# Performance work log

Hardware: AMD Instinct MI355X
Metric: run time of the kernel (lower is better)

## Reference

```python
import jax, jax.numpy as jnp
import numpy as np

V, DM, DEPTH, N = 50257, 512, 8, 16  # vocab, dim, depth, ssm_dim
B, L = 2, 1024
GATE = 0.5  # fixed_gate=True blend


def layer_norm(x, g, b):
    mu = x.mean(-1, keepdims=True)
    xm = x - mu
    var = (xm * xm).mean(-1, keepdims=True)
    return xm * jax.lax.rsqrt(var + 1e-5) * g + b


def ssm(u, W_dt, b_dt, W_B, W_C, A_log, D_p):
    # selective SSM: h_t = exp(dt_t*A)*h_{t-1} + dt_t*B_t*u_t ; y_t = C_t.h_t + D*u_t
    dt = jax.nn.softplus(u @ W_dt + b_dt)            # (B,L,DM)
    Bm = u @ W_B                                      # (B,L,N)
    Cm = u @ W_C                                      # (B,L,N)
    A = -jnp.exp(A_log)                               # (DM,N), stable (negative)

    def step(h, inp):
        dt_t, B_t, C_t, u_t = inp                     # (B,DM),(B,N),(B,N),(B,DM)
        h = jnp.exp(dt_t[..., None] * A) * h + (dt_t * u_t)[..., None] * B_t[:, None, :]
        y = jnp.einsum('bdn,bn->bd', h, C_t)
        return h, y

    h0 = jnp.zeros((u.shape[0], DM, N), u.dtype)
    xs = (dt.transpose(1, 0, 2), Bm.transpose(1, 0, 2), Cm.transpose(1, 0, 2), u.transpose(1, 0, 2))
    _, ys = jax.lax.scan(step, h0, xs)
    return ys.transpose(1, 0, 2) + D_p * u


def wkv(x, W_r, W_k, W_v, W_o, t_decay, t_first):
    # RWKV-4 channel-wise WKV recurrence
    r = jax.nn.sigmoid(x @ W_r)
    k = jnp.clip(x @ W_k, -30.0, 30.0)
    v = x @ W_v
    w = jnp.exp(-jnp.exp(t_decay))                    # (DM,) decay in (0,1)

    def step(carry, inp):
        a, b = carry
        k_t, v_t = inp
        ek = jnp.exp(k_t)
        eu = jnp.exp(t_first + k_t)
        out = (a + eu * v_t) / (b + eu + 1e-6)
        return (w * a + ek * v_t, w * b + ek), out

    a0 = jnp.zeros((x.shape[0], DM), x.dtype)
    _, o = jax.lax.scan(step, (a0, jnp.zeros_like(a0)), (k.transpose(1, 0, 2), v.transpose(1, 0, 2)))
    return (r * o.transpose(1, 0, 2)) @ W_o


def setup_inputs() -> dict:
    key = jax.random.key(0)
    ks = jax.random.split(key, 16)
    s = 0.02
    inp = {
        'input_ids': jax.random.randint(ks[0], (B, L), 0, V, dtype=jnp.int32),
        'emb': jax.random.normal(ks[1], (V, DM), jnp.float32) * s,
        'ln1_g': jnp.ones((DEPTH, DM), jnp.float32),
        'ln1_b': jnp.zeros((DEPTH, DM), jnp.float32),
        'W_dt': jax.random.normal(ks[2], (DEPTH, DM, DM), jnp.float32) * s,
        'b_dt': jnp.zeros((DEPTH, DM), jnp.float32),
        'W_B': jax.random.normal(ks[3], (DEPTH, DM, N), jnp.float32) * s,
        'W_C': jax.random.normal(ks[4], (DEPTH, DM, N), jnp.float32) * s,
        'A_log': jnp.broadcast_to(jnp.log(jnp.arange(1, N + 1, dtype=jnp.float32)), (DEPTH, DM, N)).copy(),
        'D_p': jnp.ones((DEPTH, DM), jnp.float32),
        'ln2_g': jnp.ones((DEPTH, DM), jnp.float32),
        'ln2_b': jnp.zeros((DEPTH, DM), jnp.float32),
        'W_r': jax.random.normal(ks[5], (DEPTH, DM, DM), jnp.float32) * s,
        'W_k': jax.random.normal(ks[6], (DEPTH, DM, DM), jnp.float32) * s,
        'W_v': jax.random.normal(ks[7], (DEPTH, DM, DM), jnp.float32) * s,
        'W_o': jax.random.normal(ks[8], (DEPTH, DM, DM), jnp.float32) * s,
        't_decay': jax.random.normal(ks[9], (DEPTH, DM), jnp.float32) * 0.5,
        't_first': jax.random.normal(ks[10], (DEPTH, DM), jnp.float32) * 0.5,
        'lnf_g': jnp.ones((DM,), jnp.float32),
        'lnf_b': jnp.zeros((DM,), jnp.float32),
    }
    return inp


def reference(input_ids, emb, ln1_g, ln1_b, W_dt, b_dt, W_B, W_C, A_log, D_p,
              ln2_g, ln2_b, W_r, W_k, W_v, W_o, t_decay, t_first, lnf_g, lnf_b):
    x = emb[input_ids]                                # (B,L,DM)
    for i in range(DEPTH):
        x = x + GATE * ssm(layer_norm(x, ln1_g[i], ln1_b[i]),
                           W_dt[i], b_dt[i], W_B[i], W_C[i], A_log[i], D_p[i])
        x = x + GATE * wkv(layer_norm(x, ln2_g[i], ln2_b[i]),
                           W_r[i], W_k[i], W_v[i], W_o[i], t_decay[i], t_first[i])
    x = layer_norm(x, lnf_g, lnf_b)
    logits = x @ emb.T                                # tied LM head, (B,L,V)
    return logits
```

## Files before the change

kernel.cpp:

```cpp
#include <hip/hip_runtime.h>

#define DM 512
#define NST 16
#define NDEPTH 8
#define NB 2
#define NL 1024
#define MROWS 2048
#define VOCAB 50257
#define VPAD  50304
#define NCH 64
#define CLEN 16

typedef __attribute__((ext_vector_type(8))) short bf16x8;
typedef __attribute__((ext_vector_type(4))) float f32x4;
typedef __attribute__((ext_vector_type(8))) unsigned short ushort8;

#define AS1(p) ((const __attribute__((address_space(1))) void*)(p))
#define AS3(p) ((__attribute__((address_space(3))) void*)(p))

static __device__ __forceinline__ unsigned short f2bf(float f) {
  unsigned int x = __float_as_uint(f);
  unsigned int r = (x + 0x7FFFu + ((x >> 16) & 1u)) >> 16;
  return (unsigned short)r;
}

__global__ __launch_bounds__(256) void k_gather(const int* __restrict__ ids,
    const float* __restrict__ emb, float* __restrict__ x)
{
  int gid = blockIdx.x * 256 + threadIdx.x;
  int row = gid >> 7, c = (gid & 127) * 4;
  int id = ids[row];
  *(float4*)(x + (size_t)row * DM + c) = *(const float4*)(emb + (size_t)id * DM + c);
}

__global__ void k_transpose(const float* __restrict__ Wdt, const float* __restrict__ Wr,
    const float* __restrict__ Wk, const float* __restrict__ Wv, const float* __restrict__ Wo,
    unsigned short* __restrict__ Tdtbc, unsigned short* __restrict__ Trkv, unsigned short* __restrict__ To)
{
  __shared__ float tile[32][33];
  int z = blockIdx.z, layer = z / 5, f = z % 5;
  const float* src;
  unsigned short* dst;
  size_t lw = (size_t)layer * DM * DM;
  if (f == 0)      { src = Wdt + lw; dst = Tdtbc + (size_t)layer * 640 * DM; }
  else if (f == 1) { src = Wr  + lw; dst = Trkv + (size_t)layer * 3 * DM * DM; }
  else if (f == 2) { src = Wk  + lw; dst = Trkv + (size_t)layer * 3 * DM * DM + DM * DM; }
  else if (f == 3) { src = Wv  + lw; dst = Trkv + (size_t)layer * 3 * DM * DM + 2 * DM * DM; }
  else             { src = Wo  + lw; dst = To   + lw; }
  int tx = threadIdx.x, ty = threadIdx.y;
  int kb = blockIdx.y * 32, nb = blockIdx.x * 32;
  #pragma unroll
  for (int i = 0; i < 4; i++)
    tile[ty + i * 8][tx] = src[(size_t)(kb + ty + i * 8) * DM + nb + tx];
  __syncthreads();
  #pragma unroll
  for (int i = 0; i < 4; i++)
    dst[(size_t)(nb + ty + i * 8) * DM + kb + tx] = f2bf(tile[tx][ty + i * 8]);
}

__global__ __launch_bounds__(256) void k_bcpack(const float* __restrict__ WB,
    const float* __restrict__ WC, unsigned short* __restrict__ Tdtbc)
{
  int gid = blockIdx.x * 256 + threadIdx.x;
  int k = gid & 511, n = (gid >> 9) & 127, layer = gid >> 16;
  float v = 0.f;
  if (n < 16)      v = WB[((size_t)layer * DM + k) * NST + n];
  else if (n < 32) v = WC[((size_t)layer * DM + k) * NST + (n - 16)];
  Tdtbc[(size_t)layer * 640 * DM + (size_t)(512 + n) * DM + k] = f2bf(v);
}

__global__ __launch_bounds__(256) void k_embcvt(const float* __restrict__ emb,
    unsigned short* __restrict__ out)
{
  int gid = blockIdx.x * 256 + threadIdx.x;
  size_t base = (size_t)gid * 8;
  int row = (int)(base >> 9);
  ushort8 o;
  if (row < VOCAB) {
    float4 a = *(const float4*)(emb + base);
    float4 b = *(const float4*)(emb + base + 4);
    o[0]=f2bf(a.x); o[1]=f2bf(a.y); o[2]=f2bf(a.z); o[3]=f2bf(a.w);
    o[4]=f2bf(b.x); o[5]=f2bf(b.y); o[6]=f2bf(b.z); o[7]=f2bf(b.w);
  } else {
    o = (ushort8)0;
  }
  *(ushort8*)(out + base) = o;
}

__global__ __launch_bounds__(256) void k_ln(const float* __restrict__ x,
    const float* __restrict__ g, const float* __restrict__ bb,
    float* __restrict__ of, unsigned short* __restrict__ ob)
{
  const int w = threadIdx.x >> 6, l = threadIdx.x & 63;
  const int row = blockIdx.x * 4 + w;
  const float* xr = x + (size_t)row * DM + l * 8;
  float4 v0 = *(const float4*)(xr);
  float4 v1 = *(const float4*)(xr + 4);
  float s = v0.x + v0.y + v0.z + v0.w + v1.x + v1.y + v1.z + v1.w;
  float q = v0.x*v0.x + v0.y*v0.y + v0.z*v0.z + v0.w*v0.w
          + v1.x*v1.x + v1.y*v1.y + v1.z*v1.z + v1.w*v1.w;
  #pragma unroll
  for (int m = 1; m < 64; m <<= 1) { s += __shfl_xor(s, m); q += __shfl_xor(q, m); }
  const float mu = s * (1.0f / DM);
  const float var = q * (1.0f / DM) - mu * mu;
  const float rs = rsqrtf(var + 1e-5f);
  const float4 g0 = *(const float4*)(g + l * 8);
  const float4 g1 = *(const float4*)(g + l * 8 + 4);
  const float4 b0 = *(const float4*)(bb + l * 8);
  const float4 b1 = *(const float4*)(bb + l * 8 + 4);
  float y[8];
  y[0] = (v0.x - mu) * rs * g0.x + b0.x;
  y[1] = (v0.y - mu) * rs * g0.y + b0.y;
  y[2] = (v0.z - mu) * rs * g0.z + b0.z;
  y[3] = (v0.w - mu) * rs * g0.w + b0.w;
  y[4] = (v1.x - mu) * rs * g1.x + b1.x;
  y[5] = (v1.y - mu) * rs * g1.y + b1.y;
  y[6] = (v1.z - mu) * rs * g1.z + b1.z;
  y[7] = (v1.w - mu) * rs * g1.w + b1.w;
  if (of) {
    float4 o0 = {y[0], y[1], y[2], y[3]}, o1 = {y[4], y[5], y[6], y[7]};
    *(float4*)(of + (size_t)row * DM + l * 8) = o0;
    *(float4*)(of + (size_t)row * DM + l * 8 + 4) = o1;
  }
  if (ob) {
    ushort8 o;
    #pragma unroll
    for (int j = 0; j < 8; j++) o[j] = f2bf(y[j]);
    *(ushort8*)(ob + (size_t)row * DM + l * 8) = o;
  }
}

__global__ __launch_bounds__(256) void gemm_head(const unsigned short* __restrict__ A,
    const unsigned short* __restrict__ Bt, float* __restrict__ C, int N)
{
  constexpr int K = DM;
  __shared__ unsigned short lsA[128 * 32];
  __shared__ unsigned short lsB[128 * 32];
  const int t = threadIdx.x;
  const int w = t >> 6, l = t & 63;
  const int wm = (w >> 1) * 64, wn = (w & 1) * 64;
  const int per = gridDim.x >> 3;
  const int wg = ((int)blockIdx.x & 7) * per + ((int)blockIdx.x >> 3);
  const size_t bm = (size_t)(wg & 15) * 128, bn = (size_t)(wg >> 4) * 128;
  f32x4 acc[4][4] = {};
  const int r0 = t >> 2, c0 = (t & 3) * 8;
  const unsigned short* Ab = A + (bm + r0) * K + c0;
  const unsigned short* Bb = Bt + (bn + r0) * K + c0;
  const int lr = l & 15, lk = (l >> 4) * 8;
  for (int k0 = 0; k0 < K; k0 += 32) {
    __builtin_amdgcn_global_load_lds(AS1(Ab + k0),          AS3(lsA + t * 8),        16, 0, 0);
    __builtin_amdgcn_global_load_lds(AS1(Ab + 64 * K + k0), AS3(lsA + 2048 + t * 8), 16, 0, 0);
    __builtin_amdgcn_global_load_lds(AS1(Bb + k0),          AS3(lsB + t * 8),        16, 0, 0);
    __builtin_amdgcn_global_load_lds(AS1(Bb + 64 * K + k0), AS3(lsB + 2048 + t * 8), 16, 0, 0);
    asm volatile("s_waitcnt vmcnt(0)" ::: "memory");
    __syncthreads();
    bf16x8 af[4], bfr[4];
    #pragma unroll
    for (int i = 0; i < 4; i++) af[i]  = *(const bf16x8*)(lsA + (wm + i * 16 + lr) * 32 + lk);
    #pragma unroll
    for (int i = 0; i < 4; i++) bfr[i] = *(const bf16x8*)(lsB + (wn + i * 16 + lr) * 32 + lk);
    #pragma unroll
    for (int mi = 0; mi < 4; mi++)
      #pragma unroll
      for (int ni = 0; ni < 4; ni++)
        acc[mi][ni] = __builtin_amdgcn_mfma_f32_16x16x32_bf16(af[mi], bfr[ni], acc[mi][ni], 0, 0, 0);
    __syncthreads();
  }
  const int lg = l >> 4;
  #pragma unroll
  for (int mi = 0; mi < 4; mi++) {
    #pragma unroll
    for (int ni = 0; ni < 4; ni++) {
      int n = (int)bn + wn + ni * 16 + lr;
      if (n >= N) continue;
      size_t m0 = bm + wm + mi * 16 + lg * 4;
      #pragma unroll
      for (int j = 0; j < 4; j++)
        C[(m0 + j) * (size_t)N + n] = acc[mi][ni][j];
    }
  }
}

template<int EPI>
__global__ __launch_bounds__(256) void gemm64(const unsigned short* __restrict__ A,
    const unsigned short* __restrict__ Bt, float* __restrict__ C, int ldc,
    const float* __restrict__ bias, float* __restrict__ C2)
{
  constexpr int K = DM;
  __shared__ unsigned short lsA[64 * 32];
  __shared__ unsigned short lsB[128 * 32];
  const int t = threadIdx.x;
  const int w = t >> 6, l = t & 63;
  const int wm = (w >> 1) * 32, wn = (w & 1) * 64;
  const size_t bm = (size_t)blockIdx.x * 64, bn = (size_t)blockIdx.y * 128;
  f32x4 acc[2][4] = {};
  const int r0 = t >> 2, c0 = (t & 3) * 8;
  const unsigned short* Ab = A + (bm + r0) * K + c0;
  const unsigned short* Bb = Bt + (bn + r0) * K + c0;
  const int lr = l & 15, lk = (l >> 4) * 8;
  for (int k0 = 0; k0 < K; k0 += 32) {
    __builtin_amdgcn_global_load_lds(AS1(Ab + k0),          AS3(lsA + t * 8),        16, 0, 0);
    __builtin_amdgcn_global_load_lds(AS1(Bb + k0),          AS3(lsB + t * 8),        16, 0, 0);
    __builtin_amdgcn_global_load_lds(AS1(Bb + 64 * K + k0), AS3(lsB + 2048 + t * 8), 16, 0, 0);
    asm volatile("s_waitcnt vmcnt(0)" ::: "memory");
    __syncthreads();
    bf16x8 af[2], bfr[4];
    #pragma unroll
    for (int i = 0; i < 2; i++) af[i]  = *(const bf16x8*)(lsA + (wm + i * 16 + lr) * 32 + lk);
    #pragma unroll
    for (int i = 0; i < 4; i++) bfr[i] = *(const bf16x8*)(lsB + (wn + i * 16 + lr) * 32 + lk);
    #pragma unroll
    for (int mi = 0; mi < 2; mi++)
      #pragma unroll
      for (int ni = 0; ni < 4; ni++)
        acc[mi][ni] = __builtin_amdgcn_mfma_f32_16x16x32_bf16(af[mi], bfr[ni], acc[mi][ni], 0, 0, 0);
    __syncthreads();
  }
  const int lg = l >> 4;
  #pragma unroll
  for (int mi = 0; mi < 2; mi++) {
    #pragma unroll
    for (int ni = 0; ni < 4; ni++) {
      int n = (int)bn + wn + ni * 16 + lr;
      size_t m0 = bm + wm + mi * 16 + lg * 4;
      #pragma unroll
      for (int j = 0; j < 4; j++) {
        float v = acc[mi][ni][j];
        if (EPI == 0) {
          C[(m0 + j) * (size_t)ldc + n] = v;
        } else if (EPI == 2) {
          C2[(m0 + j) * (size_t)ldc + n] += 0.5f * v;
        } else {
          if (n < 512) {
            float b = v + bias[n];
            C[(m0 + j) * (size_t)512 + n] = fmaxf(b, 0.f) + log1pf(__expf(-fabsf(b)));
          } else if (n < 544) {
            C2[(m0 + j) * (size_t)32 + (n - 512)] = v;
          }
        }
      }
    }
  }
}

__global__ __launch_bounds__(256) void k_ssm1(const float* __restrict__ dt,
    const float* __restrict__ u, const float* __restrict__ BC,
    const float* __restrict__ A_log, float* __restrict__ Pb, float* __restrict__ Sb)
{
  const int t = threadIdx.x;
  const int grp = t >> 4, n = t & 15;
  const int cg = blockIdx.x & 63, ck = blockIdx.x >> 6;
  const int ch = cg * 16 + grp;
  const int b = ch >> 9, d = ch & 511;
  const float A = -__expf(A_log[d * NST + n]);
  const int t0 = ck * CLEN;
  const float* dtp = dt + ((size_t)b * NL + t0) * DM + d;
  const float* up  = u  + ((size_t)b * NL + t0) * DM + d;
  const float* bcp = BC + ((size_t)b * NL + t0) * 32 + n;
  float P = 1.f, S = 0.f;
  #pragma unroll
  for (int tt = 0; tt < CLEN; ++tt) {
    float dtv = dtp[(size_t)tt * DM];
    float uv  = up[(size_t)tt * DM];
    float Bv  = bcp[(size_t)tt * 32];
    float e = __expf(dtv * A);
    S = fmaf(e, S, dtv * uv * Bv);
    P *= e;
  }
  size_t cn = (size_t)ch * NST + n;
  Pb[cn * NCH + ck] = P;
  Sb[cn * NCH + ck] = S;
}

__global__ __launch_bounds__(256) void k_ssm2(const float* __restrict__ Pb,
    const float* __restrict__ Sb, float* __restrict__ H0)
{
  const int wid = blockIdx.x * 4 + (threadIdx.x >> 6);
  const int lane = threadIdx.x & 63;
  float coef = Pb[(size_t)wid * NCH + lane];
  float sum  = Sb[(size_t)wid * NCH + lane];
  #pragma unroll
  for (int m = 1; m < 64; m <<= 1) {
    float cr = __shfl_up(coef, m);
    float sr = __shfl_up(sum, m);
    if (lane >= m) { sum = fmaf(coef, sr, sum); coef *= cr; }
  }
  float hp = __shfl_up(sum, 1);
  H0[(size_t)wid * NCH + lane] = (lane == 0) ? 0.f : hp;
}

__global__ __launch_bounds__(256) void k_ssm3(const float* __restrict__ dt,
    const float* __restrict__ u, const float* __restrict__ BC,
    const float* __restrict__ A_log, const float* __restrict__ Dp,
    const float* __restrict__ H0, float* __restrict__ x)
{
  const int t = threadIdx.x;
  const int grp = t >> 4, n = t & 15;
  const int cg = blockIdx.x & 63, ck = blockIdx.x >> 6;
  const int ch = cg * 16 + grp;
  const int b = ch >> 9, d = ch & 511;
  const float A = -__expf(A_log[d * NST + n]);
  const float Dpv = Dp[d];
  const int t0 = ck * CLEN;
  const float* dtp = dt + ((size_t)b * NL + t0) * DM + d;
  const float* up  = u  + ((size_t)b * NL + t0) * DM + d;
  const float* bcp = BC + ((size_t)b * NL + t0) * 32 + n;
  float* xp = x + ((size_t)b * NL + t0) * DM + d;
  size_t cn = (size_t)ch * NST + n;
  float h = H0[cn * NCH + ck];
  #pragma unroll
  for (int tt = 0; tt < CLEN; ++tt) {
    float dtv = dtp[(size_t)tt * DM];
    float uv  = up[(size_t)tt * DM];
    float Bv  = bcp[(size_t)tt * 32];
    float Cv  = bcp[(size_t)tt * 32 + 16];
    float e = __expf(dtv * A);
    h = fmaf(e, h, dtv * uv * Bv);
    float p2 = h * Cv;
    p2 += __shfl_xor(p2, 1);
    p2 += __shfl_xor(p2, 2);
    p2 += __shfl_xor(p2, 4);
    p2 += __shfl_xor(p2, 8);
    if (n == 0) xp[(size_t)tt * DM] += 0.5f * (p2 + Dpv * uv);
  }
}

__global__ __launch_bounds__(256) void k_wkv1(const float* __restrict__ rkv,
    const float* __restrict__ tdec, float* __restrict__ SaB, float* __restrict__ SbB)
{
  const int gid = blockIdx.x * 256 + threadIdx.x;
  const int ch = gid & 1023, ck = gid >> 10;
  const int b = ch >> 9, d = ch & 511;
  const float w = __expf(-__expf(tdec[d]));
  const float* base = rkv + ((size_t)b * NL + ck * CLEN) * 1536;
  float Sa = 0.f, Sb = 0.f;
  #pragma unroll
  for (int tt = 0; tt < CLEN; ++tt) {
    const float* row = base + (size_t)tt * 1536;
    float kt = row[512 + d];
    kt = fminf(30.f, fmaxf(-30.f, kt));
    float vt = row[1024 + d];
    float ek = __expf(kt);
    Sa = fmaf(w, Sa, ek * vt);
    Sb = fmaf(w, Sb, ek);
  }
  SaB[(size_t)ch * NCH + ck] = Sa;
  SbB[(size_t)ch * NCH + ck] = Sb;
}

__global__ __launch_bounds__(256) void k_wkv2(const float* __restrict__ SaB,
    const float* __restrict__ SbB, const float* __restrict__ tdec,
    float* __restrict__ HaB, float* __restrict__ HbB)
{
  const int ch = blockIdx.x * 4 + (threadIdx.x >> 6);
  const int lane = threadIdx.x & 63;
  const int d = ch & 511;
  float coef = __expf(-16.f * __expf(tdec[d]));
  float sa = SaB[(size_t)ch * NCH + lane];
  float sb = SbB[(size_t)ch * NCH + lane];
  #pragma unroll
  for (int m = 1; m < 64; m <<= 1) {
    float cr  = __shfl_up(coef, m);
    float sar = __shfl_up(sa, m);
    float sbr = __shfl_up(sb, m);
    if (lane >= m) { sa = fmaf(coef, sar, sa); sb = fmaf(coef, sbr, sb); coef *= cr; }
  }
  float ha = __shfl_up(sa, 1);
  float hb = __shfl_up(sb, 1);
  HaB[(size_t)ch * NCH + lane] = (lane == 0) ? 0.f : ha;
  HbB[(size_t)ch * NCH + lane] = (lane == 0) ? 0.f : hb;
}

__global__ __launch_bounds__(256) void k_wkv3(const float* __restrict__ rkv,
    const float* __restrict__ tdec, const float* __restrict__ tfir,
    const float* __restrict__ HaB, const float* __restrict__ HbB,
    unsigned short* __restrict__ ro)
{
  const int gid = blockIdx.x * 256 + threadIdx.x;
  const int ch = gid & 1023, ck = gid >> 10;
  const int b = ch >> 9, d = ch & 511;
  const float w = __expf(-__expf(tdec[d]));
  const float tf = tfir[d];
  float a = HaB[(size_t)ch * NCH + ck];
  float bden = HbB[(size_t)ch * NCH + ck];
  const int t0 = ck * CLEN;
  const float* base = rkv + ((size_t)b * NL + t0) * 1536;
  unsigned short* rop = ro + ((size_t)b * NL + t0) * DM + d;
  #pragma unroll
  for (int tt = 0; tt < CLEN; ++tt) {
    const float* row = base + (size_t)tt * 1536;
    float rv = row[d];
    float kt = row[512 + d];
    kt = fminf(30.f, fmaxf(-30.f, kt));
    float vt = row[1024 + d];
    float ek = __expf(kt);
    float eu = __expf(tf + kt);
    float out = __fdividef(a + eu * vt, bden + eu + 1e-6f);
    float sig = __fdividef(1.f, 1.f + __expf(-rv));
    rop[(size_t)tt * DM] = f2bf(sig * out);
    a = fmaf(w, a, ek * vt);
    bden = fmaf(w, bden, ek);
  }
}

extern "C" void kernel_launch(void* const* d_in, const int* in_sizes, int n_in,
                              void* d_out, int out_size, void* d_ws, size_t ws_size,
                              hipStream_t stream)
{
  const int*   ids   = (const int*)d_in[0];
  const float* emb   = (const float*)d_in[1];
  const float* ln1_g = (const float*)d_in[2];
  const float* ln1_b = (const float*)d_in[3];
  const float* W_dt  = (const float*)d_in[4];
  const float* b_dt  = (const float*)d_in[5];
  const float* W_B   = (const float*)d_in[6];
  const float* W_C   = (const float*)d_in[7];
  const float* A_log = (const float*)d_in[8];
  const float* D_p   = (const float*)d_in[9];
  const float* ln2_g = (const float*)d_in[10];
  const float* ln2_b = (const float*)d_in[11];
  const float* W_r   = (const float*)d_in[12];
  const float* W_k   = (const float*)d_in[13];
  const float* W_v   = (const float*)d_in[14];
  const float* W_o   = (const float*)d_in[15];
  const float* t_dec = (const float*)d_in[16];
  const float* t_fir = (const float*)d_in[17];
  const float* lnf_g = (const float*)d_in[18];
  const float* lnf_b = (const float*)d_in[19];

  char* p = (char*)d_ws;
  float*          xres  = (float*)(p + 0);
  float*          u32   = (float*)(p + 4194304);
  float*          dtb   = (float*)(p + 8388608);
  float*          rkv   = (float*)(p + 12582912);
  float*          BCb   = (float*)(p + 25165824);
  unsigned short* abuf  = (unsigned short*)(p + 25427968);
  unsigned short* Tdtbc = (unsigned short*)(p + 27525120);
  unsigned short* To    = (unsigned short*)(p + 32768000);
  unsigned short* Trkv  = (unsigned short*)(p + 36962304);
  unsigned short* Tem   = (unsigned short*)(p + 49545216);

  float* Pb = rkv;
  float* Sb = rkv + 1048576;
  float* H0 = rkv + 2097152;
  float* SaB = dtb;
  float* SbB = dtb + 65536;
  float* HaB = dtb + 131072;
  float* HbB = dtb + 196608;

  k_gather<<<1024, 256, 0, stream>>>(ids, emb, xres);
  k_transpose<<<dim3(16, 16, 40), dim3(32, 8), 0, stream>>>(W_dt, W_r, W_k, W_v, W_o, Tdtbc, Trkv, To);
  k_bcpack<<<2048, 256, 0, stream>>>(W_B, W_C, Tdtbc);
  k_embcvt<<<12576, 256, 0, stream>>>(emb, Tem);

  for (int i = 0; i < NDEPTH; ++i) {
    k_ln<<<512, 256, 0, stream>>>(xres, ln1_g + i * DM, ln1_b + i * DM, u32, abuf);
    gemm64<3><<<dim3(32, 5), 256, 0, stream>>>(abuf, Tdtbc + (size_t)i * 640 * DM, dtb,
        512, b_dt + i * DM, BCb);
    k_ssm1<<<4096, 256, 0, stream>>>(dtb, u32, BCb, A_log + (size_t)i * DM * NST, Pb, Sb);
    k_ssm2<<<4096, 256, 0, stream>>>(Pb, Sb, H0);
    k_ssm3<<<4096, 256, 0, stream>>>(dtb, u32, BCb, A_log + (size_t)i * DM * NST,
        D_p + i * DM, H0, xres);
    k_ln<<<512, 256, 0, stream>>>(xres, ln2_g + i * DM, ln2_b + i * DM, nullptr, abuf);
    gemm64<0><<<dim3(32, 12), 256, 0, stream>>>(abuf, Trkv + (size_t)i * 3 * DM * DM, rkv,
        1536, nullptr, nullptr);
    k_wkv1<<<256, 256, 0, stream>>>(rkv, t_dec + i * DM, SaB, SbB);
    k_wkv2<<<256, 256, 0, stream>>>(SaB, SbB, t_dec + i * DM, HaB, HbB);
    k_wkv3<<<256, 256, 0, stream>>>(rkv, t_dec + i * DM, t_fir + i * DM, HaB, HbB, abuf);
    gemm64<2><<<dim3(32, 4), 256, 0, stream>>>(abuf, To + (size_t)i * DM * DM, nullptr,
        512, nullptr, xres);
  }

  k_ln<<<512, 256, 0, stream>>>(xres, lnf_g, lnf_b, nullptr, abuf);
  gemm_head<<<6288, 256, 0, stream>>>(abuf, Tem, (float*)d_out, VOCAB);
}
```

Measured before the change: 1.270 ms.

## Double-buffer GEMMs with swizzled LDS and fuse chunked scan kernels

Replaces the separate head and layer GEMMs with one templated kernel. It double-buffers K-tiles of 64 through LDS with an XOR swizzle and a partial vmcnt wait, so global loads overlap the MFMA work and LDS bank conflicts drop. It also fuses the per-chunk reduction and the cross-chunk warp scan for both the SSM and WKV recurrences into single kernels, which removes two launches per layer and the round-trip through intermediate buffers. The cost is higher LDS use per block and more complex wait-count bookkeeping.

```diff
diff --git a/kernel.cpp b/kernel.cpp
--- a/kernel.cpp
+++ b/kernel.cpp
@@ -130,103 +130,99 @@
   }
 }
 
-__global__ __launch_bounds__(256) void gemm_head(const unsigned short* __restrict__ A,
-    const unsigned short* __restrict__ Bt, float* __restrict__ C, int N)
+template<int BM, int EPI, bool SWZ>
+__global__ __launch_bounds__(256) void gemm2p(const unsigned short* __restrict__ A,
+    const unsigned short* __restrict__ Bt, float* __restrict__ C, int N, int ldc,
+    const float* __restrict__ bias, float* __restrict__ C2)
 {
   constexpr int K = DM;
-  __shared__ unsigned short lsA[128 * 32];
-  __shared__ unsigned short lsB[128 * 32];
+  constexpr int AOPS = BM / 32;
+  constexpr int MI = BM / 32;
+  __shared__ unsigned short lsA[2][BM * 64];
+  __shared__ unsigned short lsB[2][128 * 64];
   const int t = threadIdx.x;
   const int w = t >> 6, l = t & 63;
-  const int wm = (w >> 1) * 64, wn = (w & 1) * 64;
-  const int per = gridDim.x >> 3;
-  const int wg = ((int)blockIdx.x & 7) * per + ((int)blockIdx.x >> 3);
-  const size_t bm = (size_t)(wg & 15) * 128, bn = (size_t)(wg >> 4) * 128;
-  f32x4 acc[4][4] = {};
-  const int r0 = t >> 2, c0 = (t & 3) * 8;
-  const unsigned short* Ab = A + (bm + r0) * K + c0;
-  const unsigned short* Bb = Bt + (bn + r0) * K + c0;
-  const int lr = l & 15, lk = (l >> 4) * 8;
-  for (int k0 = 0; k0 < K; k0 += 32) {
-    __builtin_amdgcn_global_load_lds(AS1(Ab + k0),          AS3(lsA + t * 8),        16, 0, 0);
-    __builtin_amdgcn_global_load_lds(AS1(Ab + 64 * K + k0), AS3(lsA + 2048 + t * 8), 16, 0, 0);
-    __builtin_amdgcn_global_load_lds(AS1(Bb + k0),          AS3(lsB + t * 8),        16, 0, 0);
-    __builtin_amdgcn_global_load_lds(AS1(Bb + 64 * K + k0), AS3(lsB + 2048 + t * 8), 16, 0, 0);
-    asm volatile("s_waitcnt vmcnt(0)" ::: "memory");
-    __syncthreads();
-    bf16x8 af[4], bfr[4];
-    #pragma unroll
-    for (int i = 0; i < 4; i++) af[i]  = *(const bf16x8*)(lsA + (wm + i * 16 + lr) * 32 + lk);
-    #pragma unroll
-    for (int i = 0; i < 4; i++) bfr[i] = *(const bf16x8*)(lsB + (wn + i * 16 + lr) * 32 + lk);
-    #pragma unroll
-    for (int mi = 0; mi < 4; mi++)
+  const int wm = (w >> 1) * (BM / 2), wn = (w & 1) * 64;
+  size_t bm, bn;
+  if constexpr (SWZ) {
+    const int per = gridDim.x >> 3;
+    const int wg = ((int)blockIdx.x & 7) * per + ((int)blockIdx.x >> 3);
+    bm = (size_t)(wg & 15) * BM; bn = (size_t)(wg >> 4) * 128;
+  } else {
+    bm = (size_t)blockIdx.x * BM; bn = (size_t)blockIdx.y * 128;
+  }
+  f32x4 acc[MI][4] = {};
+  const int srow = t >> 3, sslot = t & 7;
+  const int gs = sslot ^ (srow & 7);
+  const unsigned short* Ag = A + (bm + srow) * K + gs * 8;
+  const unsigned short* Bg = Bt + (bn + srow) * K + gs * 8;
+  const int lr = l & 15, lq = l >> 4;
+
+  auto STAGE = [&](int buf, int kt) {
+    const int k0 = kt * 64;
+    #pragma unroll
+    for (int o = 0; o < AOPS; ++o)
+      __builtin_amdgcn_global_load_lds(AS1(Ag + (size_t)(o * 32) * K + k0),
+          AS3(&lsA[buf][(o * 32 + srow) * 64 + sslot * 8]), 16, 0, 0);
+    #pragma unroll
+    for (int o = 0; o < 4; ++o)
+      __builtin_amdgcn_global_load_lds(AS1(Bg + (size_t)(o * 32) * K + k0),
+          AS3(&lsB[buf][(o * 32 + srow) * 64 + sslot * 8]), 16, 0, 0);
+  };
+
+  STAGE(0, 0);
+  int cur = 0;
+  for (int kt = 0; kt < 8; ++kt) {
+    if (kt < 7) {
+      STAGE(cur ^ 1, kt + 1);
+      if constexpr (BM == 128) asm volatile("s_waitcnt vmcnt(8)" ::: "memory");
+      else                     asm volatile("s_waitcnt vmcnt(6)" ::: "memory");
+    } else {
+      asm volatile("s_waitcnt vmcnt(0)" ::: "memory");
+    }
+    __builtin_amdgcn_s_barrier();
+    __builtin_amdgcn_sched_barrier(0);
+    bf16x8 af[MI][2], bfr[4][2];
+    #pragma unroll
+    for (int i = 0; i < MI; ++i) {
+      int row = wm + i * 16 + lr;
       #pragma unroll
-      for (int ni = 0; ni < 4; ni++)
-        acc[mi][ni] = __builtin_amdgcn_mfma_f32_16x16x32_bf16(af[mi], bfr[ni], acc[mi][ni], 0, 0, 0);
-    __syncthreads();
-  }
+      for (int h = 0; h < 2; ++h)
+        af[i][h] = *(const bf16x8*)(&lsA[cur][row * 64 + (((h * 4 + lq) ^ (row & 7)) * 8)]);
+    }
+    #pragma unroll
+    for (int i = 0; i < 4; ++i) {
+      int row = wn + i * 16 + lr;
+      #pragma unroll
+      for (int h = 0; h < 2; ++h)
+        bfr[i][h] = *(const bf16x8*)(&lsB[cur][row * 64 + (((h * 4 + lq) ^ (row & 7)) * 8)]);
+    }
+    __builtin_amdgcn_s_setprio(1);
+    #pragma unroll
+    for (int h = 0; h < 2; ++h)
+      #pragma unroll
+      for (int mi = 0; mi < MI; ++mi)
+        #pragma unroll
+        for (int ni = 0; ni < 4; ++ni)
+          acc[mi][ni] = __builtin_amdgcn_mfma_f32_16x16x32_bf16(af[mi][h], bfr[ni][h], acc[mi][ni], 0, 0, 0);
+    __builtin_amdgcn_s_setprio(0);
+    __builtin_amdgcn_sched_barrier(0);
+    __builtin_amdgcn_s_barrier();
+    cur ^= 1;
+  }
+
   const int lg = l >> 4;
   #pragma unroll
-  for (int mi = 0; mi < 4; mi++) {
-    #pragma unroll
-    for (int ni = 0; ni < 4; ni++) {
+  for (int mi = 0; mi < MI; ++mi) {
+    #pragma unroll
+    for (int ni = 0; ni < 4; ++ni) {
       int n = (int)bn + wn + ni * 16 + lr;
-      if (n >= N) continue;
+      if (EPI == 4 && n >= N) continue;
       size_t m0 = bm + wm + mi * 16 + lg * 4;
       #pragma unroll
-      for (int j = 0; j < 4; j++)
-        C[(m0 + j) * (size_t)N + n] = acc[mi][ni][j];
-    }
-  }
-}
-
-template<int EPI>
-__global__ __launch_bounds__(256) void gemm64(const unsigned short* __restrict__ A,
-    const unsigned short* __restrict__ Bt, float* __restrict__ C, int ldc,
-    const float* __restrict__ bias, float* __restrict__ C2)
-{
-  constexpr int K = DM;
-  __shared__ unsigned short lsA[64 * 32];
-  __shared__ unsigned short lsB[128 * 32];
-  const int t = threadIdx.x;
-  const int w = t >> 6, l = t & 63;
-  const int wm = (w >> 1) * 32, wn = (w & 1) * 64;
-  const size_t bm = (size_t)blockIdx.x * 64, bn = (size_t)blockIdx.y * 128;
-  f32x4 acc[2][4] = {};
-  const int r0 = t >> 2, c0 = (t & 3) * 8;
-  const unsigned short* Ab = A + (bm + r0) * K + c0;
-  const unsigned short* Bb = Bt + (bn + r0) * K + c0;
-  const int lr = l & 15, lk = (l >> 4) * 8;
-  for (int k0 = 0; k0 < K; k0 += 32) {
-    __builtin_amdgcn_global_load_lds(AS1(Ab + k0),          AS3(lsA + t * 8),        16, 0, 0);
-    __builtin_amdgcn_global_load_lds(AS1(Bb + k0),          AS3(lsB + t * 8),        16, 0, 0);
-    __builtin_amdgcn_global_load_lds(AS1(Bb + 64 * K + k0), AS3(lsB + 2048 + t * 8), 16, 0, 0);
-    asm volatile("s_waitcnt vmcnt(0)" ::: "memory");
-    __syncthreads();
-    bf16x8 af[2], bfr[4];
-    #pragma unroll
-    for (int i = 0; i < 2; i++) af[i]  = *(const bf16x8*)(lsA + (wm + i * 16 + lr) * 32 + lk);
-    #pragma unroll
-    for (int i = 0; i < 4; i++) bfr[i] = *(const bf16x8*)(lsB + (wn + i * 16 + lr) * 32 + lk);
-    #pragma unroll
-    for (int mi = 0; mi < 2; mi++)
-      #pragma unroll
-      for (int ni = 0; ni < 4; ni++)
-        acc[mi][ni] = __builtin_amdgcn_mfma_f32_16x16x32_bf16(af[mi], bfr[ni], acc[mi][ni], 0, 0, 0);
-    __syncthreads();
-  }
-  const int lg = l >> 4;
-  #pragma unroll
-  for (int mi = 0; mi < 2; mi++) {
-    #pragma unroll
-    for (int ni = 0; ni < 4; ni++) {
-      int n = (int)bn + wn + ni * 16 + lr;
-      size_t m0 = bm + wm + mi * 16 + lg * 4;
-      #pragma unroll
-      for (int j = 0; j < 4; j++) {
+      for (int j = 0; j < 4; ++j) {
         float v = acc[mi][ni][j];
-        if (EPI == 0) {
+        if (EPI == 0 || EPI == 4) {
           C[(m0 + j) * (size_t)ldc + n] = v;
         } else if (EPI == 2) {
           C2[(m0 + j) * (size_t)ldc + n] += 0.5f * v;
@@ -243,17 +239,16 @@
   }
 }
 
-__global__ __launch_bounds__(256) void k_ssm1(const float* __restrict__ dt,
+__global__ __launch_bounds__(256) void k_ssmA(const float* __restrict__ dt,
     const float* __restrict__ u, const float* __restrict__ BC,
-    const float* __restrict__ A_log, float* __restrict__ Pb, float* __restrict__ Sb)
-{
-  const int t = threadIdx.x;
-  const int grp = t >> 4, n = t & 15;
-  const int cg = blockIdx.x & 63, ck = blockIdx.x >> 6;
-  const int ch = cg * 16 + grp;
+    const float* __restrict__ A_log, float* __restrict__ H0)
+{
+  const int wid = blockIdx.x * 4 + (threadIdx.x >> 6);
+  const int lane = threadIdx.x & 63;
+  const int ch = wid >> 4, n = wid & 15;
   const int b = ch >> 9, d = ch & 511;
   const float A = -__expf(A_log[d * NST + n]);
-  const int t0 = ck * CLEN;
+  const int t0 = lane * CLEN;
   const float* dtp = dt + ((size_t)b * NL + t0) * DM + d;
   const float* up  = u  + ((size_t)b * NL + t0) * DM + d;
   const float* bcp = BC + ((size_t)b * NL + t0) * 32 + n;
@@ -267,25 +262,13 @@
     S = fmaf(e, S, dtv * uv * Bv);
     P *= e;
   }
-  size_t cn = (size_t)ch * NST + n;
-  Pb[cn * NCH + ck] = P;
-  Sb[cn * NCH + ck] = S;
-}
-
-__global__ __launch_bounds__(256) void k_ssm2(const float* __restrict__ Pb,
-    const float* __restrict__ Sb, float* __restrict__ H0)
-{
-  const int wid = blockIdx.x * 4 + (threadIdx.x >> 6);
-  const int lane = threadIdx.x & 63;
-  float coef = Pb[(size_t)wid * NCH + lane];
-  float sum  = Sb[(size_t)wid * NCH + lane];
   #pragma unroll
   for (int m = 1; m < 64; m <<= 1) {
-    float cr = __shfl_up(coef, m);
-    float sr = __shfl_up(sum, m);
-    if (lane >= m) { sum = fmaf(coef, sr, sum); coef *= cr; }
-  }
-  float hp = __shfl_up(sum, 1);
+    float cr = __shfl_up(P, m);
+    float sr = __shfl_up(S, m);
+    if (lane >= m) { S = fmaf(P, sr, S); P *= cr; }
+  }
+  float hp = __shfl_up(S, 1);
   H0[(size_t)wid * NCH + lane] = (lane == 0) ? 0.f : hp;
 }
 
@@ -325,14 +308,14 @@
   }
 }
 
-__global__ __launch_bounds__(256) void k_wkv1(const float* __restrict__ rkv,
-    const float* __restrict__ tdec, float* __restrict__ SaB, float* __restrict__ SbB)
-{
-  const int gid = blockIdx.x * 256 + threadIdx.x;
-  const int ch = gid & 1023, ck = gid >> 10;
+__global__ __launch_bounds__(256) void k_wkvA(const float* __restrict__ rkv,
+    const float* __restrict__ tdec, float* __restrict__ HaB, float* __restrict__ HbB)
+{
+  const int ch = blockIdx.x * 4 + (threadIdx.x >> 6);
+  const int lane = threadIdx.x & 63;
   const int b = ch >> 9, d = ch & 511;
   const float w = __expf(-__expf(tdec[d]));
-  const float* base = rkv + ((size_t)b * NL + ck * CLEN) * 1536;
+  const float* base = rkv + ((size_t)b * NL + lane * CLEN) * 1536;
   float Sa = 0.f, Sb = 0.f;
   #pragma unroll
   for (int tt = 0; tt < CLEN; ++tt) {
@@ -344,29 +327,16 @@
     Sa = fmaf(w, Sa, ek * vt);
     Sb = fmaf(w, Sb, ek);
   }
-  SaB[(size_t)ch * NCH + ck] = Sa;
-  SbB[(size_t)ch * NCH + ck] = Sb;
-}
-
-__global__ __launch_bounds__(256) void k_wkv2(const float* __restrict__ SaB,
-    const float* __restrict__ SbB, const float* __restrict__ tdec,
-    float* __restrict__ HaB, float* __restrict__ HbB)
-{
-  const int ch = blockIdx.x * 4 + (threadIdx.x >> 6);
-  const int lane = threadIdx.x & 63;
-  const int d = ch & 511;
   float coef = __expf(-16.f * __expf(tdec[d]));
-  float sa = SaB[(size_t)ch * NCH + lane];
-  float sb = SbB[(size_t)ch * NCH + lane];
   #pragma unroll
   for (int m = 1; m < 64; m <<= 1) {
     float cr  = __shfl_up(coef, m);
-    float sar = __shfl_up(sa, m);
-    float sbr = __shfl_up(sb, m);
-    if (lane >= m) { sa = fmaf(coef, sar, sa); sb = fmaf(coef, sbr, sb); coef *= cr; }
-  }
-  float ha = __shfl_up(sa, 1);
-  float hb = __shfl_up(sb, 1);
+    float sar = __shfl_up(Sa, m);
+    float sbr = __shfl_up(Sb, m);
+    if (lane >= m) { Sa = fmaf(coef, sar, Sa); Sb = fmaf(coef, sbr, Sb); coef *= cr; }
+  }
+  float ha = __shfl_up(Sa, 1);
+  float hb = __shfl_up(Sb, 1);
   HaB[(size_t)ch * NCH + lane] = (lane == 0) ? 0.f : ha;
   HbB[(size_t)ch * NCH + lane] = (lane == 0) ? 0.f : hb;
 }
@@ -440,11 +410,7 @@
   unsigned short* Trkv  = (unsigned short*)(p + 36962304);
   unsigned short* Tem   = (unsigned short*)(p + 49545216);
 
-  float* Pb = rkv;
-  float* Sb = rkv + 1048576;
-  float* H0 = rkv + 2097152;
-  float* SaB = dtb;
-  float* SbB = dtb + 65536;
+  float* H0  = rkv + 2097152;
   float* HaB = dtb + 131072;
   float* HbB = dtb + 196608;
 
@@ -455,22 +421,21 @@
 
   for (int i = 0; i < NDEPTH; ++i) {
     k_ln<<<512, 256, 0, stream>>>(xres, ln1_g + i * DM, ln1_b + i * DM, u32, abuf);
-    gemm64<3><<<dim3(32, 5), 256, 0, stream>>>(abuf, Tdtbc + (size_t)i * 640 * DM, dtb,
-        512, b_dt + i * DM, BCb);
-    k_ssm1<<<4096, 256, 0, stream>>>(dtb, u32, BCb, A_log + (size_t)i * DM * NST, Pb, Sb);
-    k_ssm2<<<4096, 256, 0, stream>>>(Pb, Sb, H0);
+    gemm2p<64, 3, false><<<dim3(32, 5), 256, 0, stream>>>(abuf, Tdtbc + (size_t)i * 640 * DM,
+        dtb, 640, 512, b_dt + i * DM, BCb);
+    k_ssmA<<<4096, 256, 0, stream>>>(dtb, u32, BCb, A_log + (size_t)i * DM * NST, H0);
     k_ssm3<<<4096, 256, 0, stream>>>(dtb, u32, BCb, A_log + (size_t)i * DM * NST,
         D_p + i * DM, H0, xres);
     k_ln<<<512, 256, 0, stream>>>(xres, ln2_g + i * DM, ln2_b + i * DM, nullptr, abuf);
-    gemm64<0><<<dim3(32, 12), 256, 0, stream>>>(abuf, Trkv + (size_t)i * 3 * DM * DM, rkv,
-        1536, nullptr, nullptr);
-    k_wkv1<<<256, 256, 0, stream>>>(rkv, t_dec + i * DM, SaB, SbB);
-    k_wkv2<<<256, 256, 0, stream>>>(SaB, SbB, t_dec + i * DM, HaB, HbB);
+    gemm2p<64, 0, false><<<dim3(32, 12), 256, 0, stream>>>(abuf, Trkv + (size_t)i * 3 * DM * DM,
+        rkv, 1536, 1536, nullptr, nullptr);
+    k_wkvA<<<256, 256, 0, stream>>>(rkv, t_dec + i * DM, HaB, HbB);
     k_wkv3<<<256, 256, 0, stream>>>(rkv, t_dec + i * DM, t_fir + i * DM, HaB, HbB, abuf);
-    gemm64<2><<<dim3(32, 4), 256, 0, stream>>>(abuf, To + (size_t)i * DM * DM, nullptr,
-        512, nullptr, xres);
+    gemm2p<64, 2, false><<<dim3(32, 4), 256, 0, stream>>>(abuf, To + (size_t)i * DM * DM,
+        nullptr, 512, 512, nullptr, xres);
   }
 
   k_ln<<<512, 256, 0, stream>>>(xres, lnf_g, lnf_b, nullptr, abuf);
-  gemm_head<<<6288, 256, 0, stream>>>(abuf, Tem, (float*)d_out, VOCAB);
-}
+  gemm2p<128, 4, true><<<6288, 256, 0, stream>>>(abuf, Tem, (float*)d_out,
+      VOCAB, VOCAB, nullptr, nullptr);
+}
```

Measured after the change: 2.340 ms. +84.3%, slower.
